# Kernel optimization log

Measured on AMD Instinct MI355X. Metric: run time of the kernel, lower is better.

Reference implementation:

```python
import jax, jax.numpy as jnp
import numpy as np

LEAK = 0.01  # F.leaky_relu default negative_slope
TAU = 1.0    # sinkhorn_tau
ITERS = 5    # sinkhorn_iters


def leaky_relu(x):
    return jnp.where(x >= 0, x, LEAK * x)


def setup_inputs() -> dict:
    key = jax.random.key(0)
    B, N, F, E, H, L = 512, 200, 32, 128, 128, 2
    ks = jax.random.split(key, 8)
    def s(k, shape, fan_in):
        return jax.random.normal(k, shape, dtype=jnp.float32) * (1.0 / np.sqrt(fan_in)).astype(np.float32)
    return {
        "x": jax.random.normal(ks[0], (B, N, F), dtype=jnp.float32),
        "w_emb": s(ks[1], (E, F), F),
        "b_emb": jnp.zeros((E,), jnp.float32),
        "w_ih": s(ks[2], (L, 4 * H, E), H),   # stacked per-layer LSTM input weights
        "w_hh": s(ks[3], (L, 4 * H, H), H),   # stacked per-layer LSTM recurrent weights
        "b_ih": jnp.zeros((L, 4 * H), jnp.float32),
        "b_hh": jnp.zeros((L, 4 * H), jnp.float32),
        "w_fc1": s(ks[4], (E, H), H),
        "b_fc1": jnp.zeros((E,), jnp.float32),
        "w_fc2": s(ks[5], (N, E), E),
        "b_fc2": jnp.zeros((N,), jnp.float32),
        "do_round": 0,  # non-differentiable Hungarian rounding path disabled
    }


def _lstm_layer(xs, h0, c0, Wih, Whh, b):
    # xs: [N, B, E]  (seq-major, like torch.nn.LSTM); h0, c0: [B, H]
    def step(carry, x_t):
        h, c = carry
        g = x_t @ Wih.T + h @ Whh.T + b               # [B, 4H]
        i, f, gg, o = jnp.split(g, 4, axis=-1)        # torch gate order i,f,g,o
        c = jax.nn.sigmoid(f) * c + jax.nn.sigmoid(i) * jnp.tanh(gg)
        h = jax.nn.sigmoid(o) * jnp.tanh(c)
        return (h, c), h
    (hN, cN), hs = jax.lax.scan(step, (h0, c0), xs)
    return hs, hN, cN


def _sinkhorn(M, tau, n_iters):
    # exp(M / tau) followed by alternating row / column normalization
    x = jnp.exp(M / tau)
    for _ in range(n_iters):
        x = x / jnp.sum(x, axis=2, keepdims=True)  # row normalize
        x = x / jnp.sum(x, axis=1, keepdims=True)  # column normalize
    return x


def reference(x, w_emb, b_emb, w_ih, w_hh, b_ih, b_hh, w_fc1, b_fc1, w_fc2, b_fc2, do_round):
    # do_round=0: the Hungarian rounding branch (host round-trip) is skipped;
    # the module then returns just the Sinkhorn output psi.
    B = x.shape[0]
    H = w_hh.shape[-1]
    e = leaky_relu(x @ w_emb.T + b_emb)            # [B, N, E]
    xs = jnp.transpose(e, (1, 0, 2))               # [N, B, E]
    h = jnp.zeros((B, H), x.dtype)
    c = jnp.zeros((B, H), x.dtype)
    hs = xs
    # NB: original code feeds the SAME embedded x to every LSTM layer,
    # carrying only the (h, c) state between layers.
    for l in range(w_ih.shape[0]):
        hs, h, c = _lstm_layer(xs, h, c, w_ih[l], w_hh[l], b_ih[l] + b_hh[l])
    out = jnp.transpose(hs, (1, 0, 2))             # [B, N, H]
    out = leaky_relu(out @ w_fc1.T + b_fc1)        # [B, N, E]
    M = out @ w_fc2.T + b_fc2                      # [B, N, N]
    psi = _sinkhorn(M, TAU, ITERS)
    return psi
```

## Files before the change

kernel.cpp:

```cpp
#include <hip/hip_runtime.h>
#include <cstdint>
#include <cstddef>

#define LEAK 0.01f
#define L2E 1.4426950408889634f

typedef _Float16 f16;
typedef __attribute__((ext_vector_type(4))) _Float16 f16x4;
typedef __attribute__((ext_vector_type(8))) _Float16 f16x8;
typedef __attribute__((ext_vector_type(4))) float f32x4;
typedef __attribute__((ext_vector_type(2))) unsigned u32x2;

static __device__ __forceinline__ f16x8 pack8s(float4 a, float4 b, float s) {
  f16x8 r;
  r[0] = (f16)(a.x * s); r[1] = (f16)(a.y * s); r[2] = (f16)(a.z * s); r[3] = (f16)(a.w * s);
  r[4] = (f16)(b.x * s); r[5] = (f16)(b.y * s); r[6] = (f16)(b.z * s); r[7] = (f16)(b.w * s);
  return r;
}
static __device__ __forceinline__ f16x8 pack8(float4 a, float4 b) {
  return pack8s(a, b, 1.0f);
}
#define MFMA16(a, b, c) __builtin_amdgcn_mfma_f32_16x16x32_f16((a), (b), (c), 0, 0, 0)

static __device__ __forceinline__ void barrier_lds() {
  asm volatile("s_waitcnt lgkmcnt(0)\n\ts_barrier" ::: "memory");
}

static __device__ __forceinline__ float permswap_lo(float a, float b) {
  u32x2 r = __builtin_amdgcn_permlane32_swap(__float_as_uint(a),
                                             __float_as_uint(b), false, false);
  return __uint_as_float(r[0]);
}

__constant__ float SCG[4] = {L2E, L2E, 2.0f * L2E, L2E};

__global__ __launch_bounds__(256) void k_emb(
    const float* __restrict__ x, const float* __restrict__ wemb,
    const float* __restrict__ bemb, f16* __restrict__ e) {
  const int t = blockIdx.x, tid = threadIdx.x;
  __shared__ __align__(16) float wl[128 * 32];
  __shared__ float bl[128];
  for (int idx = tid; idx < 1024; idx += 256)
    ((float4*)wl)[idx] = ((const float4*)wemb)[idx];
  if (tid < 128) bl[tid] = bemb[tid];

  float xa[32], xb[32];
  const float* xpa = x + ((size_t)tid * 200 + t) * 32;
  const float* xpb = x + ((size_t)(tid + 256) * 200 + t) * 32;
#pragma unroll
  for (int k4 = 0; k4 < 8; ++k4) {
    float4 va = *(const float4*)(xpa + k4 * 4);
    float4 vb = *(const float4*)(xpb + k4 * 4);
    xa[k4 * 4 + 0] = va.x; xa[k4 * 4 + 1] = va.y; xa[k4 * 4 + 2] = va.z; xa[k4 * 4 + 3] = va.w;
    xb[k4 * 4 + 0] = vb.x; xb[k4 * 4 + 1] = vb.y; xb[k4 * 4 + 2] = vb.z; xb[k4 * 4 + 3] = vb.w;
  }
  __syncthreads();

  f16* ea = e + ((size_t)t * 512 + tid) * 128;
  f16* eb = e + ((size_t)t * 512 + tid + 256) * 128;
  for (int j8 = 0; j8 < 16; ++j8) {
    f16x8 oa, ob;
#pragma unroll
    for (int jj = 0; jj < 8; ++jj) {
      int j = j8 * 8 + jj;
      float aa = bl[j], ab = bl[j];
#pragma unroll
      for (int k4 = 0; k4 < 8; ++k4) {
        float4 wv = *(const float4*)&wl[j * 32 + k4 * 4];
        aa += xa[k4 * 4 + 0] * wv.x + xa[k4 * 4 + 1] * wv.y +
              xa[k4 * 4 + 2] * wv.z + xa[k4 * 4 + 3] * wv.w;
        ab += xb[k4 * 4 + 0] * wv.x + xb[k4 * 4 + 1] * wv.y +
              xb[k4 * 4 + 2] * wv.z + xb[k4 * 4 + 3] * wv.w;
      }
      oa[jj] = (f16)(aa >= 0.f ? aa : LEAK * aa);
      ob[jj] = (f16)(ab >= 0.f ? ab : LEAK * ab);
    }
    *(f16x8*)(ea + j8 * 8) = oa;
    *(f16x8*)(eb + j8 * 8) = ob;
  }
}

static __device__ __forceinline__ void xp_waves(
    const f16* __restrict__ e, const float* __restrict__ wih,
    const float* __restrict__ bih, const float* __restrict__ bhh,
    f16* __restrict__ xp, int t0, int wid, int ntasks, int stride, int lane) {
  const int q = lane >> 4, l16 = lane & 15;
  const int ct = wid & 7;

  f16x8 BW[4][4];
  float bias[4];
#pragma unroll
  for (int G = 0; G < 4; ++G) {
    int n = G * 128 + ct * 16 + l16;
    bias[G] = (bih[n] + bhh[n]) * SCG[G];
#pragma unroll
    for (int kc = 0; kc < 4; ++kc) {
      const float4* p = (const float4*)(wih + (size_t)n * 128 + kc * 32 + q * 8);
      BW[G][kc] = pack8s(p[0], p[1], SCG[G]);
    }
  }
  for (int task = wid; task < ntasks; task += stride) {
    int g2 = task >> 3;
    int tl = g2 >> 2, btg = g2 & 3;
#pragma unroll
    for (int p = 0; p < 8; ++p) {
      int bt = btg * 8 + p;
      const f16* A = e + ((size_t)(t0 + tl) * 512 + bt * 16 + l16) * 128 + q * 8;
      f16x8 af[4];
#pragma unroll
      for (int kc = 0; kc < 4; ++kc) af[kc] = *(const f16x8*)(A + kc * 32);
      f32x4 acc[4];
#pragma unroll
      for (int G = 0; G < 4; ++G)
        acc[G] = (f32x4){bias[G], bias[G], bias[G], bias[G]};
#pragma unroll
      for (int kc = 0; kc < 4; ++kc)
#pragma unroll
        for (int G = 0; G < 4; ++G)
          acc[G] = MFMA16(af[kc], BW[G][kc], acc[G]);
      f16x8 oA, oB;
#pragma unroll
      for (int r = 0; r < 4; ++r) {
        oA[r]     = (f16)acc[0][r];
        oA[4 + r] = (f16)acc[1][r];
        oB[r]     = (f16)acc[2][r];
        oB[4 + r] = (f16)acc[3][r];
      }
      f16* dst = xp + (size_t)tl * 262144 + bt * 8192 + ct * 1024 + lane * 16;
      *(f16x8*)dst = oA;
      *(f16x8*)(dst + 8) = oB;
    }
  }
}

__global__ __launch_bounds__(256, 2) void k_xp(
    const f16* __restrict__ e, const float* __restrict__ wih,
    const float* __restrict__ bih, const float* __restrict__ bhh,
    f16* __restrict__ xp, int t0) {
  const int nt = gridDim.x * 4;
  xp_waves(e, wih, bih, bhh, xp, t0,
           blockIdx.x * 4 + (threadIdx.x >> 6), nt, nt, threadIdx.x & 63);
}

static __device__ __forceinline__ void xp_lds_layer(
    const f16* e_lds, const float* __restrict__ wih,
    const float* __restrict__ bih, const float* __restrict__ bhh,
    f16* __restrict__ xp, int tl, int ct, int lane) {
  const int q = lane >> 4, l16 = lane & 15;
  f16x8 BW[4][4];
  float bias[4];
#pragma unroll
  for (int G = 0; G < 4; ++G) {
    int n = G * 128 + ct * 16 + l16;
    bias[G] = (bih[n] + bhh[n]) * SCG[G];
#pragma unroll
    for (int kc = 0; kc < 4; ++kc) {
      const float4* p = (const float4*)(wih + (size_t)n * 128 + kc * 32 + q * 8);
      BW[G][kc] = pack8s(p[0], p[1], SCG[G]);
    }
  }
  for (int bt = 0; bt < 32; ++bt) {
    f16x8 af[4];
#pragma unroll
    for (int kc = 0; kc < 4; ++kc)
      af[kc] = *(const f16x8*)&e_lds[(bt * 16 + l16) * 136 + kc * 32 + q * 8];
    f32x4 acc[4];
#pragma unroll
    for (int G = 0; G < 4; ++G)
      acc[G] = (f32x4){bias[G], bias[G], bias[G], bias[G]};
#pragma unroll
    for (int kc = 0; kc < 4; ++kc)
#pragma unroll
      for (int G = 0; G < 4; ++G)
        acc[G] = MFMA16(af[kc], BW[G][kc], acc[G]);
    f16x8 oA, oB;
#pragma unroll
    for (int r = 0; r < 4; ++r) {
      oA[r]     = (f16)acc[0][r];
      oA[4 + r] = (f16)acc[1][r];
      oB[r]     = (f16)acc[2][r];
      oB[4 + r] = (f16)acc[3][r];
    }
    f16* dst = xp + (size_t)tl * 262144 + bt * 8192 + ct * 1024 + lane * 16;
    *(f16x8*)dst = oA;
    *(f16x8*)(dst + 8) = oB;
  }
}

static __device__ void embxp_block(
    const float* __restrict__ x, const float* __restrict__ wemb,
    const float* __restrict__ bemb,
    const float* __restrict__ wih0, const float* __restrict__ bih0,
    const float* __restrict__ bhh0, f16* __restrict__ xp0, int tl0,
    const float* __restrict__ wih1, const float* __restrict__ bih1,
    const float* __restrict__ bhh1, f16* __restrict__ xp1, int tl1,
    int t, char* smem) {
  f16* e_lds = (f16*)smem;
  float* wl  = (float*)(smem + 139264);
  float* bl  = (float*)(smem + 155648);
  const int tid = threadIdx.x;
  for (int idx = tid; idx < 1024; idx += 512)
    ((float4*)wl)[idx] = ((const float4*)wemb)[idx];
  if (tid < 128) bl[tid] = bemb[tid];

  float xr[32];
  const float* xptr = x + ((size_t)tid * 200 + t) * 32;
#pragma unroll
  for (int k4 = 0; k4 < 8; ++k4) {
    float4 v = *(const float4*)(xptr + k4 * 4);
    xr[k4 * 4 + 0] = v.x; xr[k4 * 4 + 1] = v.y;
    xr[k4 * 4 + 2] = v.z; xr[k4 * 4 + 3] = v.w;
  }
  __syncthreads();

  for (int j8 = 0; j8 < 16; ++j8) {
    f16x8 o;
#pragma unroll
    for (int jj = 0; jj < 8; ++jj) {
      int j = j8 * 8 + jj;
      float a = bl[j];
#pragma unroll
      for (int k4 = 0; k4 < 8; ++k4) {
        float4 wv = *(const float4*)&wl[j * 32 + k4 * 4];
        a += xr[k4 * 4 + 0] * wv.x + xr[k4 * 4 + 1] * wv.y +
             xr[k4 * 4 + 2] * wv.z + xr[k4 * 4 + 3] * wv.w;
      }
      o[jj] = (f16)(a >= 0.f ? a : LEAK * a);
    }
    *(f16x8*)&e_lds[tid * 136 + j8 * 8] = o;
  }
  __syncthreads();

  const int w = tid >> 6, lane = tid & 63;
  xp_lds_layer(e_lds, wih0, bih0, bhh0, xp0, tl0, w, lane);
  if (xp1) xp_lds_layer(e_lds, wih1, bih1, bhh1, xp1, tl1, w, lane);
}

__global__ __launch_bounds__(512, 2) void k_embxp(
    const float* __restrict__ x, const float* __restrict__ wemb,
    const float* __restrict__ bemb,
    const float* __restrict__ wih0, const float* __restrict__ bih0,
    const float* __restrict__ bhh0,
    const float* __restrict__ wih1, const float* __restrict__ bih1,
    const float* __restrict__ bhh1,
    f16* __restrict__ bufA, f16* __restrict__ bufB, f16* __restrict__ bufC) {
  extern __shared__ char smem[];
  const int t = blockIdx.x;
  f16* xp0 = (t < 100) ? bufA : bufB;
  int tl0 = (t < 100) ? t : t - 100;
  f16* xp1 = (t < 100) ? bufC : nullptr;
  embxp_block(x, wemb, bemb, wih0, bih0, bhh0, xp0, tl0,
              wih1, bih1, bhh1, xp1, (t < 100) ? t : 0, t, smem);
}

static __device__ __forceinline__ void rec_body(
    const f16* __restrict__ xp, const float* __restrict__ whh,
    float* __restrict__ hws, float* __restrict__ cws,
    f16* __restrict__ hs, int layer, int t0, int CH, f16* hlds, int bt) {
  const int tid = threadIdx.x;
  const int w = tid >> 6, lane = tid & 63, q = lane >> 4, l16 = lane & 15;
  const int row0 = (q & 1) * 4 + (q >> 1) * 2;

  f16x8 BH[4][4];
#pragma unroll
  for (int G = 0; G < 4; ++G) {
    int n = G * 128 + w * 16 + l16;
#pragma unroll
    for (int kc = 0; kc < 4; ++kc) {
      const float4* ph = (const float4*)(whh + (size_t)n * 128 + kc * 32 + q * 8);
      BH[G][kc] = pack8s(ph[0], ph[1], SCG[G]);
    }
  }

  float cst0, cst1;
  if (layer == 0 && t0 == 0) {
    cst0 = 0.f; cst1 = 0.f;
    for (int idx = tid; idx < 8 * 136; idx += 512)
      hlds[8 * 136 + idx] = (f16)0.f;
  } else {
    const float* cp = cws + ((size_t)(bt * 8 + w) * 64 + lane) * 2;
    cst0 = cp[0]; cst1 = cp[1];
    const float* hp = hws + ((size_t)(bt * 8 + w) * 64 + lane) * 2;
    hlds[(8 + row0 + 0) * 136 + w * 16 + l16] = (f16)hp[0];
    hlds[(8 + row0 + 1) * 136 + w * 16 + l16] = (f16)hp[1];
  }
  barrier_lds();

  const int qo = (bt & 1) * 2 + (q & 1);
  const f16* xpl = xp + (((size_t)(bt >> 1) * 8 + w) * 64 + qo * 16 + l16) * 16;
  f16x8 xa = *(const f16x8*)(xpl);
  f16x8 xb = *(const f16x8*)(xpl + 8);
  const int t1 = (CH > 1) ? 1 : 0;
  f16x8 n1a = *(const f16x8*)(xpl + (size_t)t1 * 262144);
  f16x8 n1b = *(const f16x8*)(xpl + (size_t)t1 * 262144 + 8);

  float hk0 = 0.f, hk1 = 0.f;
  for (int tl = 0; tl < CH; ++tl) {
    int tn2 = (tl + 2 < CH) ? tl + 2 : CH - 1;
    const f16* xpn = xpl + (size_t)tn2 * 262144;
    f16x8 n2a = *(const f16x8*)(xpn);
    f16x8 n2b = *(const f16x8*)(xpn + 8);

    const int rb = (tl + 1) & 1;
    f16x8 ah[4];
#pragma unroll
    for (int kc = 0; kc < 4; ++kc)
      ah[kc] = *(const f16x8*)&hlds[(rb * 8 + (l16 & 7)) * 136 + kc * 32 + q * 8];

    f32x4 acc[4];
#pragma unroll
    for (int r = 0; r < 4; ++r) {
      acc[0][r] = (float)xa[r];
      acc[1][r] = (float)xa[4 + r];
      acc[2][r] = (float)xb[r];
      acc[3][r] = (float)xb[4 + r];
    }
#pragma unroll
    for (int kc = 0; kc < 4; ++kc)
#pragma unroll
      for (int G = 0; G < 4; ++G)
        acc[G] = MFMA16(ah[kc], BH[G][kc], acc[G]);

    float e0[4], e1[4];
#pragma unroll
    for (int G = 0; G < 4; ++G) {
      e0[G] = permswap_lo(acc[G][0], acc[G][2]);
      e1[G] = permswap_lo(acc[G][1], acc[G][3]);
    }

    const int wb = tl & 1;
    f16 h16_0, h16_1;
#pragma unroll
    for (int j = 0; j < 2; ++j) {
      float gi = j ? e1[0] : e0[0];
      float gf = j ? e1[1] : e0[1];
      float gg = j ? e1[2] : e0[2];
      float go = j ? e1[3] : e0[3];
      float cprev = j ? cst1 : cst0;
      float ui = __builtin_amdgcn_exp2f(-gi);
      float uf = __builtin_amdgcn_exp2f(-gf);
      float ug = __builtin_amdgcn_exp2f(-fmaxf(gg, -88.f));
      float uo = __builtin_amdgcn_exp2f(-go);
      float sf = __builtin_amdgcn_rcpf(1.0f + uf);
      float p1 = (1.0f - ug) * __builtin_amdgcn_rcpf((1.0f + ui) * (1.0f + ug));
      float cc = sf * cprev + p1;
      if (j) cst1 = cc; else cst0 = cc;
      float ccl = fminf(fmaxf(cc, -30.f), 30.f) * (-2.0f * L2E);
      float ucc = __builtin_amdgcn_exp2f(ccl);
      float hv = (1.0f - ucc) * __builtin_amdgcn_rcpf((1.0f + uo) * (1.0f + ucc));
      if (j) { hk1 = hv; h16_1 = (f16)hv; } else { hk0 = hv; h16_0 = (f16)hv; }
      hlds[(wb * 8 + row0 + j) * 136 + w * 16 + l16] = j ? h16_1 : h16_0;
    }
    if (layer != 0) {
      f16* hp0 = hs + ((size_t)(bt * 8 + row0) * 200 + (t0 + tl)) * 128 + w * 16 + l16;
      hp0[0] = h16_0;
      hp0[25600] = h16_1;
    }
    barrier_lds();
    xa = n1a; xb = n1b; n1a = n2a; n1b = n2b;
  }

  float* hp = hws + ((size_t)(bt * 8 + w) * 64 + lane) * 2;
  hp[0] = hk0; hp[1] = hk1;
  float* cp = cws + ((size_t)(bt * 8 + w) * 64 + lane) * 2;
  cp[0] = cst0; cp[1] = cst1;
}

__global__ __launch_bounds__(512, 2) void k_rec(
    const f16* __restrict__ xp, const float* __restrict__ whh,
    float* __restrict__ hws, float* __restrict__ cws,
    f16* __restrict__ hs, int layer, int t0, int CH) {
  extern __shared__ char smem[];
  rec_body(xp, whh, hws, cws, hs, layer, t0, CH, (f16*)smem, blockIdx.x);
}

__global__ __launch_bounds__(512, 2) void k_recxp2(
    const f16* __restrict__ xp_r, const float* __restrict__ whh,
    float* __restrict__ hws, float* __restrict__ cws, f16* __restrict__ hs,
    const float* __restrict__ x, const float* __restrict__ wemb,
    const float* __restrict__ bemb,
    const float* __restrict__ wih1, const float* __restrict__ bih1,
    const float* __restrict__ bhh1, f16* __restrict__ xp_w) {
  extern __shared__ char smem[];
  if (blockIdx.x < 64) {
    rec_body(xp_r, whh, hws, cws, hs, 0, 100, 100, (f16*)smem, blockIdx.x);
  } else {
    int t = 100 + (blockIdx.x - 64);
    embxp_block(x, wemb, bemb, wih1, bih1, bhh1, xp_w, t - 100,
                nullptr, nullptr, nullptr, nullptr, 0, t, smem);
  }
}

__global__ __launch_bounds__(512, 4) void k_head(
    const f16* __restrict__ hs, const float* __restrict__ wfc1,
    const float* __restrict__ bfc1, const float* __restrict__ wfc2,
    const float* __restrict__ bfc2, float* __restrict__ psi) {
  extern __shared__ char smem[];
  f16* E = (f16*)smem;
  f16* o1 = (f16*)(smem + 27200);
  float* uu = (float*)(smem + 80000);
  float* vv = (float*)(smem + 80800);
  const int b = blockIdx.x, tid = threadIdx.x;
  const int w = tid >> 6, lane = tid & 63, q = lane >> 4, l16 = lane & 15;
  const f16* A = hs + (size_t)b * 200 * 128;

  f16x8 BF1[4];
  float bias1;
  {
    int n = w * 16 + l16;
    bias1 = bfc1[n];
#pragma unroll
    for (int kc = 0; kc < 4; ++kc) {
      const float4* p = (const float4*)(wfc1 + (size_t)n * 128 + kc * 32 + q * 8);
      BF1[kc] = pack8(p[0], p[1]);
    }
  }
  f16x8 BF2[2][4];
  float bias2[2] = {0.f, 0.f};
#pragma unroll
  for (int ci = 0; ci < 2; ++ci) {
    int ct = w + ci * 8;
    if (ct < 13) {
      int n = ct * 16 + l16; if (n > 199) n = 199;
      bias2[ci] = bfc2[n];
#pragma unroll
      for (int kc = 0; kc < 4; ++kc) {
        const float4* p = (const float4*)(wfc2 + (size_t)n * 128 + kc * 32 + q * 8);
        BF2[ci][kc] = pack8(p[0], p[1]);
      }
    }
  }

  for (int rt = 0; rt < 13; ++rt) {
    int m = rt * 16 + l16; if (m > 199) m = 199;
    f16x8 af[4];
#pragma unroll
    for (int kc = 0; kc < 4; ++kc)
      af[kc] = *(const f16x8*)(A + (size_t)m * 128 + kc * 32 + q * 8);
    f32x4 acc = (f32x4){bias1, bias1, bias1, bias1};
#pragma unroll
    for (int kc = 0; kc < 4; ++kc) acc = MFMA16(af[kc], BF1[kc], acc);
    int col = w * 16 + l16;
#pragma unroll
    for (int r = 0; r < 4; ++r) {
      int row = rt * 16 + q * 4 + r;
      float vvv = acc[r]; vvv = vvv >= 0.f ? vvv : LEAK * vvv;
      if (row < 200) o1[row * 136 + col] = (f16)vvv;
    }
  }
  __syncthreads();

  for (int rt = 0; rt < 13; ++rt) {
    int m = rt * 16 + l16; if (m > 199) m = 199;
    f16x8 af[4];
#pragma unroll
    for (int kc = 0; kc < 4; ++kc)
      af[kc] = *(const f16x8*)&o1[m * 136 + kc * 32 + q * 8];
    __syncthreads();
#pragma unroll
    for (int ci = 0; ci < 2; ++ci) {
      int ct = w + ci * 8;
      if (ct < 13) {
        f32x4 acc = (f32x4){bias2[ci], bias2[ci], bias2[ci], bias2[ci]};
#pragma unroll
        for (int kc = 0; kc < 4; ++kc) acc = MFMA16(af[kc], BF2[ci][kc], acc);
        int col = ct * 16 + l16;
#pragma unroll
        for (int r = 0; r < 4; ++r) {
          int row = rt * 16 + q * 4 + r;
          if (row < 200 && col < 200) E[row * 200 + col] = (f16)__expf(acc[r]);
        }
      }
    }
  }
  __syncthreads();
  if (tid < 200) vv[tid] = 1.0f;
  __syncthreads();

  for (int it = 0; it < 5; ++it) {
    if (tid < 400) {
      int r = tid >> 1, h = tid & 1;
      const f16* Er = E + r * 200 + h * 100;
      const float* vp = vv + h * 100;
      float s0 = 0.f, s1 = 0.f;
      for (int j = 0; j < 100; j += 4) {
        f16x4 e4 = *(const f16x4*)(Er + j);
        float4 v4 = *(const float4*)(vp + j);
        s0 += (float)e4[0] * v4.x + (float)e4[1] * v4.y;
        s1 += (float)e4[2] * v4.z + (float)e4[3] * v4.w;
      }
      float s = s0 + s1;
      s += __shfl_xor(s, 1);
      if (h == 0) uu[r] = __builtin_amdgcn_rcpf(s);
    }
    __syncthreads();
    if (tid < 400) {
      int c4 = tid >> 3, g = tid & 7;
      const f16* Ec = E + (size_t)(g * 25) * 200 + c4 * 4;
      float a0 = 0.f, a1 = 0.f, a2 = 0.f, a3 = 0.f;
      for (int i = 0; i < 25; ++i) {
        f16x4 e4 = *(const f16x4*)(Ec + i * 200);
        float ui = uu[g * 25 + i];
        a0 += (float)e4[0] * ui;
        a1 += (float)e4[1] * ui;
        a2 += (float)e4[2] * ui;
        a3 += (float)e4[3] * ui;
      }
#pragma unroll
      for (int mk = 1; mk <= 4; mk <<= 1) {
        a0 += __shfl_xor(a0, mk);
        a1 += __shfl_xor(a1, mk);
        a2 += __shfl_xor(a2, mk);
        a3 += __shfl_xor(a3, mk);
      }
      if (g == 0) {
        float4 o;
        o.x = __builtin_amdgcn_rcpf(a0);
        o.y = __builtin_amdgcn_rcpf(a1);
        o.z = __builtin_amdgcn_rcpf(a2);
        o.w = __builtin_amdgcn_rcpf(a3);
        *(float4*)(vv + c4 * 4) = o;
      }
    }
    __syncthreads();
  }

  float* P = psi + (size_t)b * 40000;
  for (int idx4 = tid; idx4 < 10000; idx4 += 512) {
    unsigned i = ((unsigned)idx4 * 5243u) >> 18;
    unsigned jq = (unsigned)idx4 - i * 50u;
    f16x4 e4 = *(const f16x4*)(E + i * 200 + jq * 4);
    float4 v4 = *(const float4*)(vv + jq * 4);
    float ui = uu[i];
    float4 o;
    o.x = ui * (float)e4[0] * v4.x;
    o.y = ui * (float)e4[1] * v4.y;
    o.z = ui * (float)e4[2] * v4.z;
    o.w = ui * (float)e4[3] * v4.w;
    *(float4*)(P + i * 200 + jq * 4) = o;
  }
}

extern "C" void kernel_launch(void* const* d_in, const int* in_sizes, int n_in,
                              void* d_out, int out_size, void* d_ws, size_t ws_size,
                              hipStream_t stream) {
  const float* x    = (const float*)d_in[0];
  const float* wemb = (const float*)d_in[1];
  const float* bemb = (const float*)d_in[2];
  const float* wih  = (const float*)d_in[3];
  const float* whh  = (const float*)d_in[4];
  const float* bih  = (const float*)d_in[5];
  const float* bhh  = (const float*)d_in[6];
  const float* wfc1 = (const float*)d_in[7];
  const float* bfc1 = (const float*)d_in[8];
  const float* wfc2 = (const float*)d_in[9];
  const float* bfc2 = (const float*)d_in[10];
  float* psi = (float*)d_out;

  char* ws = (char*)d_ws;
  const float* wih1 = wih + 65536;  const float* whh1 = whh + 65536;
  const float* bih1 = bih + 512;    const float* bhh1 = bhh + 512;

  (void)hipFuncSetAttribute((const void*)k_head,
                            hipFuncAttributeMaxDynamicSharedMemorySize, 81600);

  const bool pipelined = (ws_size >= 157810688ull);

  if (pipelined) {
    f16* bufA = (f16*)(ws);
    f16* bufB = (f16*)(ws + 52428800);
    f16* bufC = (f16*)(ws + 104857600);
    float* hws = (float*)(ws + 157286400);
    float* cws = (float*)(ws + 157548544);
    f16* hs = bufB;

    (void)hipFuncSetAttribute((const void*)k_embxp,
                              hipFuncAttributeMaxDynamicSharedMemorySize, 156160);
    (void)hipFuncSetAttribute((const void*)k_recxp2,
                              hipFuncAttributeMaxDynamicSharedMemorySize, 156160);

    k_embxp<<<200, 512, 156160, stream>>>(x, wemb, bemb,
                                          wih, bih, bhh, wih1, bih1, bhh1,
                                          bufA, bufB, bufC);
    k_rec<<<64, 512, 4608, stream>>>(bufA, whh, hws, cws, hs, 0, 0, 100);
    k_recxp2<<<164, 512, 156160, stream>>>(bufB, whh, hws, cws, hs,
                                           x, wemb, bemb,
                                           wih1, bih1, bhh1, bufA);
    k_rec<<<64, 512, 4608, stream>>>(bufC, whh1, hws, cws, hs, 1, 0, 100);
    k_rec<<<64, 512, 4608, stream>>>(bufA, whh1, hws, cws, hs, 1, 100, 100);

    k_head<<<512, 512, 81600, stream>>>(hs, wfc1, bfc1, wfc2, bfc2, psi);
  } else {
    f16*   e   = (f16*)(ws);
    float* hws = (float*)(ws + 26214400);
    float* cws = (float*)(ws + 26476544);
    f16*   hs  = (f16*)(ws + 26738688);
    f16*   xpA = (f16*)(ws + 52953088);
    const size_t fixed = 52953088;
    const int cands[] = {100, 50, 40, 25, 20, 10, 8, 5, 4, 2, 1};
    int CH = 1;
    for (int ci = 0; ci < 11; ++ci) {
      if (fixed + (size_t)cands[ci] * 524288 <= ws_size) { CH = cands[ci]; break; }
    }
    k_emb<<<200, 256, 0, stream>>>(x, wemb, bemb, e);
    for (int l = 0; l < 2; ++l) {
      const float* wih_l = wih + (size_t)l * 65536;
      const float* whh_l = whh + (size_t)l * 65536;
      const float* bih_l = bih + (size_t)l * 512;
      const float* bhh_l = bhh + (size_t)l * 512;
      for (int t0 = 0; t0 < 200; t0 += CH) {
        k_xp<<<CH * 8, 256, 0, stream>>>(e, wih_l, bih_l, bhh_l, xpA, t0);
        k_rec<<<64, 512, 4608, stream>>>(xpA, whh_l, hws, cws, hs, l, t0, CH);
      }
    }
    k_head<<<512, 512, 81600, stream>>>(hs, wfc1, bfc1, wfc2, bfc2, psi);
  }
}
```

Baseline: 562.9 us.

## Split embed+input-projection into half-batch blocks and overlap more with recurrence

Each embedding plus input-projection block now handles half the batch, which cuts LDS use so more blocks fit per CU. The first launch now covers only layer-0 inputs for the first 100 timesteps. The remaining layer-0 and layer-1 projections are moved into kernels that run alongside the recurrent blocks. This aims to hide the projection work behind the latency-bound recurrence, at the risk of the extra blocks contending for CUs with the recurrent blocks.

```diff
diff --git a/kernel.cpp b/kernel.cpp
--- a/kernel.cpp
+++ b/kernel.cpp
@@ -142,10 +142,10 @@
            blockIdx.x * 4 + (threadIdx.x >> 6), nt, nt, threadIdx.x & 63);
 }
 
-static __device__ __forceinline__ void xp_lds_layer(
+static __device__ __forceinline__ void xp_half(
     const f16* e_lds, const float* __restrict__ wih,
     const float* __restrict__ bih, const float* __restrict__ bhh,
-    f16* __restrict__ xp, int tl, int ct, int lane) {
+    f16* __restrict__ xp, int tl, int half, int ct, int lane) {
   const int q = lane >> 4, l16 = lane & 15;
   f16x8 BW[4][4];
   float bias[4];
@@ -159,7 +159,7 @@
       BW[G][kc] = pack8s(p[0], p[1], SCG[G]);
     }
   }
-  for (int bt = 0; bt < 32; ++bt) {
+  for (int bt = 0; bt < 16; ++bt) {
     f16x8 af[4];
 #pragma unroll
     for (int kc = 0; kc < 4; ++kc)
@@ -181,76 +181,77 @@
       oB[r]     = (f16)acc[2][r];
       oB[4 + r] = (f16)acc[3][r];
     }
-    f16* dst = xp + (size_t)tl * 262144 + bt * 8192 + ct * 1024 + lane * 16;
+    f16* dst = xp + (size_t)tl * 262144 + (half * 16 + bt) * 8192 + ct * 1024 + lane * 16;
     *(f16x8*)dst = oA;
     *(f16x8*)(dst + 8) = oB;
   }
 }
 
-static __device__ void embxp_block(
+static __device__ void embxp_half(
     const float* __restrict__ x, const float* __restrict__ wemb,
     const float* __restrict__ bemb,
-    const float* __restrict__ wih0, const float* __restrict__ bih0,
-    const float* __restrict__ bhh0, f16* __restrict__ xp0, int tl0,
-    const float* __restrict__ wih1, const float* __restrict__ bih1,
-    const float* __restrict__ bhh1, f16* __restrict__ xp1, int tl1,
-    int t, char* smem) {
+    const float* __restrict__ wih, const float* __restrict__ bih,
+    const float* __restrict__ bhh, f16* __restrict__ xp,
+    int tl, int t, int half, char* smem) {
   f16* e_lds = (f16*)smem;
-  float* wl  = (float*)(smem + 139264);
-  float* bl  = (float*)(smem + 155648);
+  float* wl  = (float*)(smem + 69632);
+  float* bl  = (float*)(smem + 86016);
   const int tid = threadIdx.x;
   for (int idx = tid; idx < 1024; idx += 512)
     ((float4*)wl)[idx] = ((const float4*)wemb)[idx];
   if (tid < 128) bl[tid] = bemb[tid];
 
-  float xr[32];
-  const float* xptr = x + ((size_t)tid * 200 + t) * 32;
-#pragma unroll
-  for (int k4 = 0; k4 < 8; ++k4) {
-    float4 v = *(const float4*)(xptr + k4 * 4);
-    xr[k4 * 4 + 0] = v.x; xr[k4 * 4 + 1] = v.y;
-    xr[k4 * 4 + 2] = v.z; xr[k4 * 4 + 3] = v.w;
+  float xa[32], xb[32];
+  if (tid < 128) {
+    const float* xpa = x + ((size_t)(half * 256 + tid) * 200 + t) * 32;
+    const float* xpb = x + ((size_t)(half * 256 + tid + 128) * 200 + t) * 32;
+#pragma unroll
+    for (int k4 = 0; k4 < 8; ++k4) {
+      float4 va = *(const float4*)(xpa + k4 * 4);
+      float4 vb = *(const float4*)(xpb + k4 * 4);
+      xa[k4 * 4 + 0] = va.x; xa[k4 * 4 + 1] = va.y; xa[k4 * 4 + 2] = va.z; xa[k4 * 4 + 3] = va.w;
+      xb[k4 * 4 + 0] = vb.x; xb[k4 * 4 + 1] = vb.y; xb[k4 * 4 + 2] = vb.z; xb[k4 * 4 + 3] = vb.w;
+    }
   }
   __syncthreads();
 
-  for (int j8 = 0; j8 < 16; ++j8) {
-    f16x8 o;
-#pragma unroll
-    for (int jj = 0; jj < 8; ++jj) {
-      int j = j8 * 8 + jj;
-      float a = bl[j];
-#pragma unroll
-      for (int k4 = 0; k4 < 8; ++k4) {
-        float4 wv = *(const float4*)&wl[j * 32 + k4 * 4];
-        a += xr[k4 * 4 + 0] * wv.x + xr[k4 * 4 + 1] * wv.y +
-             xr[k4 * 4 + 2] * wv.z + xr[k4 * 4 + 3] * wv.w;
-      }
-      o[jj] = (f16)(a >= 0.f ? a : LEAK * a);
-    }
-    *(f16x8*)&e_lds[tid * 136 + j8 * 8] = o;
+  if (tid < 128) {
+    f16* ea = e_lds + tid * 136;
+    f16* eb = e_lds + (tid + 128) * 136;
+    for (int j8 = 0; j8 < 16; ++j8) {
+      f16x8 oa, ob;
+#pragma unroll
+      for (int jj = 0; jj < 8; ++jj) {
+        int j = j8 * 8 + jj;
+        float aa = bl[j], ab = bl[j];
+#pragma unroll
+        for (int k4 = 0; k4 < 8; ++k4) {
+          float4 wv = *(const float4*)&wl[j * 32 + k4 * 4];
+          aa += xa[k4 * 4 + 0] * wv.x + xa[k4 * 4 + 1] * wv.y +
+                xa[k4 * 4 + 2] * wv.z + xa[k4 * 4 + 3] * wv.w;
+          ab += xb[k4 * 4 + 0] * wv.x + xb[k4 * 4 + 1] * wv.y +
+                xb[k4 * 4 + 2] * wv.z + xb[k4 * 4 + 3] * wv.w;
+        }
+        oa[jj] = (f16)(aa >= 0.f ? aa : LEAK * aa);
+        ob[jj] = (f16)(ab >= 0.f ? ab : LEAK * ab);
+      }
+      *(f16x8*)(ea + j8 * 8) = oa;
+      *(f16x8*)(eb + j8 * 8) = ob;
+    }
   }
   __syncthreads();
 
-  const int w = tid >> 6, lane = tid & 63;
-  xp_lds_layer(e_lds, wih0, bih0, bhh0, xp0, tl0, w, lane);
-  if (xp1) xp_lds_layer(e_lds, wih1, bih1, bhh1, xp1, tl1, w, lane);
-}
-
-__global__ __launch_bounds__(512, 2) void k_embxp(
+  xp_half(e_lds, wih, bih, bhh, xp, tl, half, tid >> 6, tid & 63);
+}
+
+__global__ __launch_bounds__(512, 2) void k_embxpA(
     const float* __restrict__ x, const float* __restrict__ wemb,
     const float* __restrict__ bemb,
     const float* __restrict__ wih0, const float* __restrict__ bih0,
-    const float* __restrict__ bhh0,
-    const float* __restrict__ wih1, const float* __restrict__ bih1,
-    const float* __restrict__ bhh1,
-    f16* __restrict__ bufA, f16* __restrict__ bufB, f16* __restrict__ bufC) {
+    const float* __restrict__ bhh0, f16* __restrict__ bufA) {
   extern __shared__ char smem[];
-  const int t = blockIdx.x;
-  f16* xp0 = (t < 100) ? bufA : bufB;
-  int tl0 = (t < 100) ? t : t - 100;
-  f16* xp1 = (t < 100) ? bufC : nullptr;
-  embxp_block(x, wemb, bemb, wih0, bih0, bhh0, xp0, tl0,
-              wih1, bih1, bhh1, xp1, (t < 100) ? t : 0, t, smem);
+  int t = blockIdx.x >> 1, half = blockIdx.x & 1;
+  embxp_half(x, wemb, bemb, wih0, bih0, bhh0, bufA, t, t, half, smem);
 }
 
 static __device__ __forceinline__ void rec_body(
@@ -374,20 +375,28 @@
   rec_body(xp, whh, hws, cws, hs, layer, t0, CH, (f16*)smem, blockIdx.x);
 }
 
-__global__ __launch_bounds__(512, 2) void k_recxp2(
+__global__ __launch_bounds__(512, 2) void k_recshadow(
     const f16* __restrict__ xp_r, const float* __restrict__ whh,
     float* __restrict__ hws, float* __restrict__ cws, f16* __restrict__ hs,
+    int layer_r, int t0_r,
     const float* __restrict__ x, const float* __restrict__ wemb,
     const float* __restrict__ bemb,
-    const float* __restrict__ wih1, const float* __restrict__ bih1,
-    const float* __restrict__ bhh1, f16* __restrict__ xp_w) {
+    const float* __restrict__ wihA, const float* __restrict__ bihA,
+    const float* __restrict__ bhhA, f16* __restrict__ xpA, int tbaseA, int nA,
+    const float* __restrict__ wihB, const float* __restrict__ bihB,
+    const float* __restrict__ bhhB, f16* __restrict__ xpB, int tbaseB) {
   extern __shared__ char smem[];
   if (blockIdx.x < 64) {
-    rec_body(xp_r, whh, hws, cws, hs, 0, 100, 100, (f16*)smem, blockIdx.x);
+    rec_body(xp_r, whh, hws, cws, hs, layer_r, t0_r, 100, (f16*)smem, blockIdx.x);
   } else {
-    int t = 100 + (blockIdx.x - 64);
-    embxp_block(x, wemb, bemb, wih1, bih1, bhh1, xp_w, t - 100,
-                nullptr, nullptr, nullptr, nullptr, 0, t, smem);
+    int j = blockIdx.x - 64;
+    const float *wih, *bih, *bhh;
+    f16* xpo;
+    int tb;
+    if (j < nA) { wih = wihA; bih = bihA; bhh = bhhA; xpo = xpA; tb = tbaseA; }
+    else { j -= nA; wih = wihB; bih = bihB; bhh = bhhB; xpo = xpB; tb = tbaseB; }
+    int t = tb + (j >> 1), half = j & 1;
+    embxp_half(x, wemb, bemb, wih, bih, bhh, xpo, t - tb, t, half, smem);
   }
 }
 
@@ -574,18 +583,20 @@
     float* cws = (float*)(ws + 157548544);
     f16* hs = bufB;
 
-    (void)hipFuncSetAttribute((const void*)k_embxp,
-                              hipFuncAttributeMaxDynamicSharedMemorySize, 156160);
-    (void)hipFuncSetAttribute((const void*)k_recxp2,
-                              hipFuncAttributeMaxDynamicSharedMemorySize, 156160);
-
-    k_embxp<<<200, 512, 156160, stream>>>(x, wemb, bemb,
-                                          wih, bih, bhh, wih1, bih1, bhh1,
-                                          bufA, bufB, bufC);
-    k_rec<<<64, 512, 4608, stream>>>(bufA, whh, hws, cws, hs, 0, 0, 100);
-    k_recxp2<<<164, 512, 156160, stream>>>(bufB, whh, hws, cws, hs,
-                                           x, wemb, bemb,
-                                           wih1, bih1, bhh1, bufA);
+    (void)hipFuncSetAttribute((const void*)k_embxpA,
+                              hipFuncAttributeMaxDynamicSharedMemorySize, 86528);
+    (void)hipFuncSetAttribute((const void*)k_recshadow,
+                              hipFuncAttributeMaxDynamicSharedMemorySize, 86528);
+
+    k_embxpA<<<200, 512, 86528, stream>>>(x, wemb, bemb, wih, bih, bhh, bufA);
+    k_recshadow<<<464, 512, 86528, stream>>>(bufA, whh, hws, cws, hs, 0, 0,
+        x, wemb, bemb,
+        wih, bih, bhh, bufB, 100, 200,
+        wih1, bih1, bhh1, bufC, 0);
+    k_recshadow<<<264, 512, 86528, stream>>>(bufB, whh, hws, cws, hs, 0, 100,
+        x, wemb, bemb,
+        wih1, bih1, bhh1, bufA, 100, 200,
+        wih1, bih1, bhh1, bufA, 100);
     k_rec<<<64, 512, 4608, stream>>>(bufC, whh1, hws, cws, hs, 1, 0, 100);
     k_rec<<<64, 512, 4608, stream>>>(bufA, whh1, hws, cws, hs, 1, 100, 100);
 
```

Result: slower. 613.3 us (+9.0%).
